# Kernel optimization log

Hardware: AMD Instinct MI355X
Metric: run time of the kernel (lower is better)

## Reference

```python
import jax, jax.numpy as jnp
import numpy as np

N_CLASSES = 9
N_GROUPS = 2


def setup_inputs() -> dict:
    key = jax.random.key(0)
    k1, k2 = jax.random.split(key)
    N = 16_777_216  # number of samples
    preds = jax.random.randint(k1, (N,), 0, N_CLASSES, dtype=jnp.int32)
    attrs = jax.random.randint(k2, (N,), 0, N_GROUPS, dtype=jnp.int32)
    return {"preds": preds, "attrs": attrs}


def reference(preds, attrs):
    # Fused histogram: flatten (class, group) -> single bin id in [0, 18)
    flat = preds * N_GROUPS + attrs  # [N]
    counts = jax.ops.segment_sum(
        jnp.ones_like(flat, dtype=jnp.float32), flat,
        num_segments=N_CLASSES * N_GROUPS,
    ).reshape(N_CLASSES, N_GROUPS)  # [9, 2] histogram

    n_attr_1 = jnp.sum(attrs != 0).astype(jnp.float32)
    n_attr_0 = jnp.float32(attrs.shape[0]) - n_attr_1

    diff = counts[:, 0] / n_attr_0 - counts[:, 1] / n_attr_1  # [9]
    return jnp.sum(diff * diff)
```

## Files before the change

### kernel.cpp

```cpp
#include <hip/hip_runtime.h>


#define N_CLASSES 9
#define N_GROUPS 2
#define NBINS (N_CLASSES * N_GROUPS)
#define ITEMS 8
#define BDIM 512

typedef int vint4 __attribute__((ext_vector_type(4)));

__global__ __launch_bounds__(BDIM, 3) void spd_hist_kernel(
    const int* __restrict__ preds,
    const int* __restrict__ attrs,
    unsigned int* __restrict__ partials,
    int n4, int n)
{
    __shared__ unsigned int lh0[N_CLASSES];
    __shared__ unsigned int lh1[N_CLASSES];
    if (threadIdx.x < N_CLASSES) { lh0[threadIdx.x] = 0u; lh1[threadIdx.x] = 0u; }
    __syncthreads();

    unsigned int cnt[N_CLASSES];
    #pragma unroll
    for (int p = 0; p < N_CLASSES; ++p) cnt[p] = 0u;

    const vint4* __restrict__ p4 = (const vint4*)preds;
    const vint4* __restrict__ a4 = (const vint4*)attrs;

    const int span = BDIM * ITEMS;
    for (int S = blockIdx.x * span; S < n4; S += gridDim.x * span) {
        const int s = S + (int)threadIdx.x;
        unsigned long long accT = 0ull, acc1 = 0ull;

        if (S + span <= n4) {
            vint4 P0, P1, P2, P3, P4, P5, P6, P7;
            vint4 A0, A1, A2, A3, A4, A5, A6, A7;
            #define LD(i) P##i = p4[s + i * BDIM]; A##i = a4[s + i * BDIM];
            LD(0) LD(1) LD(2) LD(3) LD(4) LD(5) LD(6) LD(7)
            #undef LD
            asm volatile("" :
                "+v"(P0), "+v"(P1), "+v"(P2), "+v"(P3),
                "+v"(P4), "+v"(P5), "+v"(P6), "+v"(P7),
                "+v"(A0), "+v"(A1), "+v"(A2), "+v"(A3),
                "+v"(A4), "+v"(A5), "+v"(A6), "+v"(A7));

            #define CONSUME(i) { \
                { unsigned long long inc = 1ull << (7 * P##i.x); accT += inc; acc1 += (A##i.x == 0) ? 0ull : inc; } \
                { unsigned long long inc = 1ull << (7 * P##i.y); accT += inc; acc1 += (A##i.y == 0) ? 0ull : inc; } \
                { unsigned long long inc = 1ull << (7 * P##i.z); accT += inc; acc1 += (A##i.z == 0) ? 0ull : inc; } \
                { unsigned long long inc = 1ull << (7 * P##i.w); accT += inc; acc1 += (A##i.w == 0) ? 0ull : inc; } \
            }
            CONSUME(0) CONSUME(1) CONSUME(2) CONSUME(3)
            CONSUME(4) CONSUME(5) CONSUME(6) CONSUME(7)
            #undef CONSUME
        } else {
            for (int k = 0; k < ITEMS; ++k) {
                const int idx = s + k * BDIM;
                if (idx < n4) {
                    vint4 pp = p4[idx];
                    vint4 aa = a4[idx];
                    {
                        unsigned long long inc = 1ull << (7 * pp.x);
                        accT += inc; acc1 += (aa.x == 0) ? 0ull : inc;
                    }
                    {
                        unsigned long long inc = 1ull << (7 * pp.y);
                        accT += inc; acc1 += (aa.y == 0) ? 0ull : inc;
                    }
                    {
                        unsigned long long inc = 1ull << (7 * pp.z);
                        accT += inc; acc1 += (aa.z == 0) ? 0ull : inc;
                    }
                    {
                        unsigned long long inc = 1ull << (7 * pp.w);
                        accT += inc; acc1 += (aa.w == 0) ? 0ull : inc;
                    }
                }
            }
        }

        #pragma unroll
        for (int p = 0; p < N_CLASSES; ++p) {
            unsigned int ct = (unsigned int)(accT >> (7 * p)) & 127u;
            unsigned int c1 = (unsigned int)(acc1 >> (7 * p)) & 127u;
            cnt[p] += (ct - c1) | (c1 << 16);
        }
    }

    if (blockIdx.x == 0) {
        for (int t = n4 * 4 + (int)threadIdx.x; t < n; t += BDIM)
            cnt[preds[t]] += (attrs[t] == 0) ? 1u : 0x10000u;
    }

    #pragma unroll
    for (int m = 1; m < 64; m <<= 1) {
        #pragma unroll
        for (int p = 0; p < N_CLASSES; ++p)
            cnt[p] += __shfl_xor(cnt[p], m, 64);
    }

    if ((threadIdx.x & 63) == 0) {
        #pragma unroll
        for (int p = 0; p < N_CLASSES; ++p) {
            atomicAdd(&lh0[p], cnt[p] & 0xFFFFu);
            atomicAdd(&lh1[p], cnt[p] >> 16);
        }
    }
    __syncthreads();

    if (threadIdx.x < NBINS) {
        int c = threadIdx.x >> 1;
        unsigned int v = (threadIdx.x & 1) ? lh1[c] : lh0[c];
        partials[blockIdx.x * NBINS + threadIdx.x] = v;
    }
}

__global__ __launch_bounds__(1024) void spd_finalize_kernel(
    const unsigned int* __restrict__ partials,
    float* __restrict__ out, int nblocks, double n_total)
{
    __shared__ double counts[NBINS];
    const int tid = threadIdx.x;

    if (tid < NBINS * 32) {
        const int bin = tid >> 5;
        const int j = tid & 31;
        unsigned int s = 0u;
        #pragma unroll 8
        for (int b = j; b < nblocks; b += 32)
            s += partials[b * NBINS + bin];
        #pragma unroll
        for (int m = 1; m < 32; m <<= 1)
            s += __shfl_xor(s, m, 32);
        if (j == 0) counts[bin] = (double)s;
    }
    __syncthreads();

    if (tid == 0) {
        double n1 = 0.0;
        #pragma unroll
        for (int c = 0; c < N_CLASSES; ++c)
            n1 += counts[c * N_GROUPS + 1];
        double n0 = n_total - n1;
        double acc = 0.0;
        #pragma unroll
        for (int c = 0; c < N_CLASSES; ++c) {
            double d = counts[c * N_GROUPS] / n0 - counts[c * N_GROUPS + 1] / n1;
            acc += d * d;
        }
        out[0] = (float)acc;
    }
}

extern "C" void kernel_launch(void* const* d_in, const int* in_sizes, int n_in,
                              void* d_out, int out_size, void* d_ws, size_t ws_size,
                              hipStream_t stream)
{
    const int* preds = (const int*)d_in[0];
    const int* attrs = (const int*)d_in[1];
    const int n = in_sizes[0];

    unsigned int* partials = (unsigned int*)d_ws;

    const int n4 = n / 4;
    const int block = BDIM;
    const int per_block = block * ITEMS;
    int grid = (n4 + per_block - 1) / per_block;
    if (grid > 2048) grid = 2048;
    int max_grid = (int)(ws_size / (NBINS * sizeof(unsigned int)));
    if (grid > max_grid) grid = max_grid;
    if (grid < 1) grid = 1;

    spd_hist_kernel<<<grid, block, 0, stream>>>(preds, attrs, partials, n4, n);
    spd_finalize_kernel<<<1, 1024, 0, stream>>>(partials, (float*)d_out, grid, (double)n);
}
```

Baseline: 147.5 us.

## Double-buffer vector loads across four sub-tiles per block iteration

```diff
diff --git a/kernel.cpp b/kernel.cpp
--- a/kernel.cpp
+++ b/kernel.cpp
@@ -4,12 +4,15 @@
 #define N_CLASSES 9
 #define N_GROUPS 2
 #define NBINS (N_CLASSES * N_GROUPS)
-#define ITEMS 8
 #define BDIM 512
+#define ITEMS 4
+#define NITER 4
+#define SPAN (BDIM * ITEMS)
+#define BLOCKSPAN (SPAN * NITER)
 
 typedef int vint4 __attribute__((ext_vector_type(4)));
 
-__global__ __launch_bounds__(BDIM, 3) void spd_hist_kernel(
+__global__ __launch_bounds__(BDIM, 4) void spd_hist_kernel(
     const int* __restrict__ preds,
     const int* __restrict__ attrs,
     unsigned int* __restrict__ partials,
@@ -27,35 +30,50 @@
     const vint4* __restrict__ p4 = (const vint4*)preds;
     const vint4* __restrict__ a4 = (const vint4*)attrs;
 
-    const int span = BDIM * ITEMS;
-    for (int S = blockIdx.x * span; S < n4; S += gridDim.x * span) {
+    for (int S = blockIdx.x * BLOCKSPAN; S < n4; S += gridDim.x * BLOCKSPAN) {
         const int s = S + (int)threadIdx.x;
         unsigned long long accT = 0ull, acc1 = 0ull;
 
-        if (S + span <= n4) {
-            vint4 P0, P1, P2, P3, P4, P5, P6, P7;
-            vint4 A0, A1, A2, A3, A4, A5, A6, A7;
-            #define LD(i) P##i = p4[s + i * BDIM]; A##i = a4[s + i * BDIM];
-            LD(0) LD(1) LD(2) LD(3) LD(4) LD(5) LD(6) LD(7)
-            #undef LD
-            asm volatile("" :
-                "+v"(P0), "+v"(P1), "+v"(P2), "+v"(P3),
-                "+v"(P4), "+v"(P5), "+v"(P6), "+v"(P7),
-                "+v"(A0), "+v"(A1), "+v"(A2), "+v"(A3),
-                "+v"(A4), "+v"(A5), "+v"(A6), "+v"(A7));
+        if (S + BLOCKSPAN <= n4) {
+            vint4 aP0, aP1, aP2, aP3, aA0, aA1, aA2, aA3;
+            vint4 bP0, bP1, bP2, bP3, bA0, bA1, bA2, bA3;
 
-            #define CONSUME(i) { \
-                { unsigned long long inc = 1ull << (7 * P##i.x); accT += inc; acc1 += (A##i.x == 0) ? 0ull : inc; } \
-                { unsigned long long inc = 1ull << (7 * P##i.y); accT += inc; acc1 += (A##i.y == 0) ? 0ull : inc; } \
-                { unsigned long long inc = 1ull << (7 * P##i.z); accT += inc; acc1 += (A##i.z == 0) ? 0ull : inc; } \
-                { unsigned long long inc = 1ull << (7 * P##i.w); accT += inc; acc1 += (A##i.w == 0) ? 0ull : inc; } \
+            #define LDBUF(B, base) \
+                B##P0 = p4[(base)];            B##A0 = a4[(base)]; \
+                B##P1 = p4[(base) + BDIM];     B##A1 = a4[(base) + BDIM]; \
+                B##P2 = p4[(base) + 2*BDIM];   B##A2 = a4[(base) + 2*BDIM]; \
+                B##P3 = p4[(base) + 3*BDIM];   B##A3 = a4[(base) + 3*BDIM];
+
+            #define PIN(B) asm volatile("" : \
+                "+v"(B##P0), "+v"(B##P1), "+v"(B##P2), "+v"(B##P3), \
+                "+v"(B##A0), "+v"(B##A1), "+v"(B##A2), "+v"(B##A3) :: "memory");
+
+            #define CONS1(P, A) { \
+                { unsigned long long inc = 1ull << (7 * P.x); accT += inc; acc1 += (A.x == 0) ? 0ull : inc; } \
+                { unsigned long long inc = 1ull << (7 * P.y); accT += inc; acc1 += (A.y == 0) ? 0ull : inc; } \
+                { unsigned long long inc = 1ull << (7 * P.z); accT += inc; acc1 += (A.z == 0) ? 0ull : inc; } \
+                { unsigned long long inc = 1ull << (7 * P.w); accT += inc; acc1 += (A.w == 0) ? 0ull : inc; } \
             }
-            CONSUME(0) CONSUME(1) CONSUME(2) CONSUME(3)
-            CONSUME(4) CONSUME(5) CONSUME(6) CONSUME(7)
-            #undef CONSUME
+            #define CONSBUF(B) \
+                CONS1(B##P0, B##A0) CONS1(B##P1, B##A1) \
+                CONS1(B##P2, B##A2) CONS1(B##P3, B##A3)
+
+            LDBUF(a, s)
+            LDBUF(b, s + SPAN)
+            PIN(a) CONSBUF(a)
+            LDBUF(a, s + 2 * SPAN)
+            PIN(b) CONSBUF(b)
+            LDBUF(b, s + 3 * SPAN)
+            PIN(a) CONSBUF(a)
+            PIN(b) CONSBUF(b)
+
+            #undef LDBUF
+            #undef PIN
+            #undef CONS1
+            #undef CONSBUF
         } else {
-            for (int k = 0; k < ITEMS; ++k) {
-                const int idx = s + k * BDIM;
+            for (int m = 0; m < NITER * ITEMS; ++m) {
+                const int idx = s + m * BDIM;
                 if (idx < n4) {
                     vint4 pp = p4[idx];
                     vint4 aa = a4[idx];
@@ -163,14 +181,12 @@
     unsigned int* partials = (unsigned int*)d_ws;
 
     const int n4 = n / 4;
-    const int block = BDIM;
-    const int per_block = block * ITEMS;
-    int grid = (n4 + per_block - 1) / per_block;
-    if (grid > 2048) grid = 2048;
+    int grid = (n4 + BLOCKSPAN - 1) / BLOCKSPAN;
+    if (grid > 1024) grid = 1024;
     int max_grid = (int)(ws_size / (NBINS * sizeof(unsigned int)));
     if (grid > max_grid) grid = max_grid;
     if (grid < 1) grid = 1;
 
-    spd_hist_kernel<<<grid, block, 0, stream>>>(preds, attrs, partials, n4, n);
+    spd_hist_kernel<<<grid, BDIM, 0, stream>>>(preds, attrs, partials, n4, n);
     spd_finalize_kernel<<<1, 1024, 0, stream>>>(partials, (float*)d_out, grid, (double)n);
 }
```

Result: no change. 150.2 us (+1.8%).
